# Performance work log

Measured on AMD Instinct MI355X. Metric: run time of the kernel, lower is better.

Reference implementation:

```python
import jax, jax.numpy as jnp
import numpy as np

N = 8192
F_IN = 128
F_OUT = 128
NEG_SLOPE = 0.2


def setup_inputs() -> dict:
    key = jax.random.key(0)
    k_h, k_adj, k_W, k_a = jax.random.split(key, 4)
    h = jax.random.normal(k_h, (N, F_IN), dtype=jnp.float32)
    # binary adjacency mask as float (the module multiplies scores by adj)
    adj = (jax.random.uniform(k_adj, (N, N)) < 0.05).astype(jnp.float32)
    # nn.Linear(in, out, bias=False): weight shape [out, in]
    W = jax.random.normal(k_W, (F_OUT, F_IN), dtype=jnp.float32) / np.sqrt(F_IN)
    # nn.Linear(2*out, 1, bias=False): weight shape [1, 2*out]
    a = jax.random.normal(k_a, (1, 2 * F_OUT), dtype=jnp.float32) / np.sqrt(2 * F_OUT)
    return {"h": h, "adj": adj, "W": W, "a": a}


def reference(h, adj, W, a):
    # Wh: [N, F_out]
    Wh = h @ W.T
    f = Wh.shape[-1]
    # a([Wh_i ; Wh_j]) factored: e[i, j] = leaky_relu(Wh[i]@a1 + Wh[j]@a2)
    a1 = a[0, :f]  # [F_out]
    a2 = a[0, f:]  # [F_out]
    s_i = Wh @ a1  # [N]
    s_j = Wh @ a2  # [N]
    e = jax.nn.leaky_relu(s_i[:, None] + s_j[None, :], NEG_SLOPE)  # [N, N]
    # faithful to original: softmax over dim=1 of e * adj (multiplicative mask)
    attention = jax.nn.softmax(e * adj, axis=1)  # [N, N]
    return attention @ Wh  # [N, F_out]
```

## Files before the change

kernel.cpp:

```cpp
#include <hip/hip_runtime.h>

#define N_NODES 8192
#define FDIM 128
#define NEG_SLOPE 0.2f
#define SEG 512

__global__ __launch_bounds__(256) void wh_fused_kernel(
    const float* __restrict__ h, const float* __restrict__ W,
    float* __restrict__ Wh, float* __restrict__ S) {
  __shared__ float Wt[FDIM * 132];
  __shared__ float rows[32 * 132];
  const int t = threadIdx.x;
  const int base = blockIdx.x * 32;
  for (int it = 0; it < 64; ++it) {
    int idx = t + 256 * it;
    int o = idx >> 7, k = idx & 127;
    Wt[k * 132 + o] = W[idx];
  }
  for (int it = 0; it < 16; ++it) {
    int idx = t + 256 * it;
    int r = idx >> 7, col = idx & 127;
    rows[r * 132 + col] = h[(size_t)base * FDIM + idx];
  }
  __syncthreads();
  const int c4 = (t & 31) * 4;
  const int g = t >> 5;
  float acc[4][4];
#pragma unroll
  for (int rr = 0; rr < 4; ++rr)
#pragma unroll
    for (int cc = 0; cc < 4; ++cc) acc[rr][cc] = 0.f;
  for (int k = 0; k < FDIM; ++k) {
    float4 wv = *(const float4*)&Wt[k * 132 + c4];
    float rv[4];
#pragma unroll
    for (int rr = 0; rr < 4; ++rr) rv[rr] = rows[(4 * g + rr) * 132 + k];
#pragma unroll
    for (int rr = 0; rr < 4; ++rr) {
      acc[rr][0] += rv[rr] * wv.x;
      acc[rr][1] += rv[rr] * wv.y;
      acc[rr][2] += rv[rr] * wv.z;
      acc[rr][3] += rv[rr] * wv.w;
    }
  }
#pragma unroll
  for (int rr = 0; rr < 4; ++rr) {
    int r = base + 4 * g + rr;
    *(float4*)&Wh[(size_t)r * FDIM + c4] =
        make_float4(acc[rr][0], acc[rr][1], acc[rr][2], acc[rr][3]);
  }
  __syncthreads();
  float4 cs = make_float4(acc[0][0] + acc[1][0] + acc[2][0] + acc[3][0],
                          acc[0][1] + acc[1][1] + acc[2][1] + acc[3][1],
                          acc[0][2] + acc[1][2] + acc[2][2] + acc[3][2],
                          acc[0][3] + acc[1][3] + acc[2][3] + acc[3][3]);
  *(float4*)&rows[g * FDIM + c4] = cs;
  __syncthreads();
  if (t < FDIM) {
    float s = 0.f;
#pragma unroll
    for (int gg = 0; gg < 8; ++gg) s += rows[gg * FDIM + t];
    atomicAdd(&S[t], s);
  }
}

__global__ __launch_bounds__(256) void scores_kernel(
    const float* __restrict__ Wh, const float* __restrict__ a,
    float* __restrict__ s1, float* __restrict__ s2) {
  const int t = threadIdx.x;
  const int lane = t & 63;
  const int wave = t >> 6;
  const int row = blockIdx.x * 4 + wave;
  float v0 = Wh[(size_t)row * FDIM + lane];
  float v1 = Wh[(size_t)row * FDIM + 64 + lane];
  float d1 = v0 * a[lane] + v1 * a[64 + lane];
  float d2 = v0 * a[FDIM + lane] + v1 * a[FDIM + 64 + lane];
  for (int off = 32; off; off >>= 1) {
    d1 += __shfl_down(d1, off);
    d2 += __shfl_down(d2, off);
  }
  if (lane == 0) { s1[row] = d1; s2[row] = d2; }
}

__global__ __launch_bounds__(256) void gat_row_kernel(
    const float* __restrict__ adj, const float* __restrict__ Wh,
    const float* __restrict__ s1, const float* __restrict__ s2,
    const float* __restrict__ S, float* __restrict__ out) {
  const int i = blockIdx.x;
  const int t = threadIdx.x;
  const int lane = t & 63;
  const int wave = t >> 6;
  __shared__ float2 pairs[4 * SEG];
  __shared__ int counts[4];
  __shared__ float red[4];
  __shared__ float red2[4];
  __shared__ float fpart[4][FDIM];

  const float s1i = s1[i];
  const float4* __restrict__ arow = (const float4*)(adj + (size_t)i * N_NODES);
  const float4* __restrict__ s2v = (const float4*)s2;
  float2* __restrict__ mypairs = pairs + wave * SEG;
  const unsigned long long lmask = (1ull << lane) - 1ull;

  int cbase = 0;
  float lmax = -1e30f;
  float4 av = arow[t], sv = s2v[t];
#pragma unroll
  for (int it = 0; it < N_NODES / 1024; ++it) {
    float4 avn, svn;
    if (it < N_NODES / 1024 - 1) {
      avn = arow[(it + 1) * 256 + t];
      svn = s2v[(it + 1) * 256 + t];
    }
    const int j4 = it * 256 + t;
    float avv[4] = {av.x, av.y, av.z, av.w};
    float svv[4] = {sv.x, sv.y, sv.z, sv.w};
    float ecand[4];
    bool pred[4];
#pragma unroll
    for (int c = 0; c < 4; ++c) {
      float e = s1i + svv[c];
      e = e > 0.f ? e : NEG_SLOPE * e;
      ecand[c] = e;
      pred[c] = (avv[c] != 0.f);
      if (pred[c]) lmax = fmaxf(lmax, e);
    }
#pragma unroll
    for (int c = 0; c < 4; ++c) {
      unsigned long long b = __ballot(pred[c]);
      if (pred[c]) {
        int pos = cbase + (int)__popcll(b & lmask);
        if (pos < SEG)
          mypairs[pos] = make_float2(ecand[c], __int_as_float(j4 * 4 + c));
      }
      cbase += (int)__popcll(b);
    }
    av = avn; sv = svn;
  }
  if (lane == 0) counts[wave] = cbase < SEG ? cbase : SEG;
  for (int off = 32; off; off >>= 1) lmax = fmaxf(lmax, __shfl_down(lmax, off));
  if (lane == 0) red[wave] = lmax;
  __syncthreads();
  const int cnt = counts[0] + counts[1] + counts[2] + counts[3];
  float m = fmaxf(fmaxf(red[0], red[1]), fmaxf(red[2], red[3]));
  if (cnt < N_NODES) m = fmaxf(m, 0.f);
  const float em = __expf(-m);
  const int mycnt = counts[wave];
  const int half = lane >> 5, lq = lane & 31;
  const float4* __restrict__ Wh4 = (const float4*)Wh;
  float ax = 0.f, ay = 0.f, az = 0.f, aw = 0.f;
  float lsum = 0.f;
  const int nit = (mycnt + 1) >> 1;
  int it = 0;
  for (; it + 1 < nit; it += 2) {
    int p0 = 2 * it + half, p1 = p0 + 2;
    float2 pr0 = mypairs[p0 < mycnt ? p0 : 0];
    float2 pr1 = mypairs[p1 < mycnt ? p1 : 0];
    int j0 = __float_as_int(pr0.y), j1 = __float_as_int(pr1.y);
    float4 v0 = Wh4[(j0 << 5) + lq];
    float4 v1 = Wh4[(j1 << 5) + lq];
    float e0 = __expf(pr0.x - m), e1 = __expf(pr1.x - m);
    bool ok0 = p0 < mycnt, ok1 = p1 < mycnt;
    float w0 = ok0 ? e0 - em : 0.f;
    float w1 = ok1 ? e1 - em : 0.f;
    lsum += (ok0 ? e0 : 0.f) + (ok1 ? e1 : 0.f);
    ax += w0 * v0.x + w1 * v1.x;
    ay += w0 * v0.y + w1 * v1.y;
    az += w0 * v0.z + w1 * v1.z;
    aw += w0 * v0.w + w1 * v1.w;
  }
  if (it < nit) {
    int p0 = 2 * it + half;
    float2 pr0 = mypairs[p0 < mycnt ? p0 : 0];
    int j0 = __float_as_int(pr0.y);
    float4 v0 = Wh4[(j0 << 5) + lq];
    float e0 = __expf(pr0.x - m);
    bool ok0 = p0 < mycnt;
    float w0 = ok0 ? e0 - em : 0.f;
    lsum += ok0 ? e0 : 0.f;
    ax += w0 * v0.x; ay += w0 * v0.y; az += w0 * v0.z; aw += w0 * v0.w;
  }
  ax += __shfl_down(ax, 32);
  ay += __shfl_down(ay, 32);
  az += __shfl_down(az, 32);
  aw += __shfl_down(aw, 32);
  for (int off = 32; off; off >>= 1) lsum += __shfl_down(lsum, off);
  if (lane == 0) red2[wave] = lsum * (1.f / 32.f);
  if (lane < 32)
    *(float4*)&fpart[wave][4 * lq] = make_float4(ax, ay, az, aw);
  __syncthreads();
  if (t < FDIM) {
    float l = red2[0] + red2[1] + red2[2] + red2[3]
              + (float)(N_NODES - cnt) * em;
    float o = (fpart[0][t] + fpart[1][t] + fpart[2][t] + fpart[3][t]
               + em * S[t]) / l;
    out[(size_t)i * FDIM + t] = o;
  }
}

extern "C" void kernel_launch(void* const* d_in, const int* in_sizes, int n_in,
                              void* d_out, int out_size, void* d_ws, size_t ws_size,
                              hipStream_t stream) {
  const float* h   = (const float*)d_in[0];
  const float* adj = (const float*)d_in[1];
  const float* W   = (const float*)d_in[2];
  const float* a   = (const float*)d_in[3];
  float* out = (float*)d_out;
  float* Wh = (float*)d_ws;
  float* s1 = Wh + (size_t)N_NODES * FDIM;
  float* s2 = s1 + N_NODES;
  float* S  = s2 + N_NODES;

  hipMemsetAsync(S, 0, FDIM * sizeof(float), stream);
  hipLaunchKernelGGL(wh_fused_kernel, dim3(N_NODES / 32), dim3(256), 0, stream,
                     h, W, Wh, S);
  hipLaunchKernelGGL(scores_kernel, dim3(N_NODES / 4), dim3(256), 0, stream,
                     Wh, a, s1, s2);
  hipLaunchKernelGGL(gat_row_kernel, dim3(N_NODES), dim3(256), 0, stream,
                     adj, Wh, s1, s2, S, out);
}
```

Measured before the change: 453.9 us.

## Compact adjacency indices first, compute scores and exps only for neighbors

The row kernel now loads all eight adjacency float4 chunks up front and compacts nonzero column indices without reading s2 for every column. Scores are then computed by gathering s2 only at compacted neighbors, exponentials are computed once per neighbor and stored in shared memory, and the aggregation loop is unrolled by four over precomputed weights. This drops the dense s2 stream and redundant exp work, at the cost of an extra pass over shared memory and scattered s2 loads.

```diff
diff --git a/kernel.cpp b/kernel.cpp
--- a/kernel.cpp
+++ b/kernel.cpp
@@ -98,46 +98,39 @@
 
   const float s1i = s1[i];
   const float4* __restrict__ arow = (const float4*)(adj + (size_t)i * N_NODES);
-  const float4* __restrict__ s2v = (const float4*)s2;
   float2* __restrict__ mypairs = pairs + wave * SEG;
   const unsigned long long lmask = (1ull << lane) - 1ull;
 
+  float4 av[8];
+#pragma unroll
+  for (int it = 0; it < 8; ++it) av[it] = arow[it * 256 + t];
   int cbase = 0;
-  float lmax = -1e30f;
-  float4 av = arow[t], sv = s2v[t];
-#pragma unroll
-  for (int it = 0; it < N_NODES / 1024; ++it) {
-    float4 avn, svn;
-    if (it < N_NODES / 1024 - 1) {
-      avn = arow[(it + 1) * 256 + t];
-      svn = s2v[(it + 1) * 256 + t];
-    }
+#pragma unroll
+  for (int it = 0; it < 8; ++it) {
     const int j4 = it * 256 + t;
-    float avv[4] = {av.x, av.y, av.z, av.w};
-    float svv[4] = {sv.x, sv.y, sv.z, sv.w};
-    float ecand[4];
-    bool pred[4];
+    float v[4] = {av[it].x, av[it].y, av[it].z, av[it].w};
 #pragma unroll
     for (int c = 0; c < 4; ++c) {
-      float e = s1i + svv[c];
-      e = e > 0.f ? e : NEG_SLOPE * e;
-      ecand[c] = e;
-      pred[c] = (avv[c] != 0.f);
-      if (pred[c]) lmax = fmaxf(lmax, e);
-    }
-#pragma unroll
-    for (int c = 0; c < 4; ++c) {
-      unsigned long long b = __ballot(pred[c]);
-      if (pred[c]) {
+      bool pred = (v[c] != 0.f);
+      unsigned long long b = __ballot(pred);
+      if (pred) {
         int pos = cbase + (int)__popcll(b & lmask);
-        if (pos < SEG)
-          mypairs[pos] = make_float2(ecand[c], __int_as_float(j4 * 4 + c));
+        if (pos < SEG) ((int*)&mypairs[pos])[1] = j4 * 4 + c;
       }
       cbase += (int)__popcll(b);
     }
-    av = avn; sv = svn;
-  }
-  if (lane == 0) counts[wave] = cbase < SEG ? cbase : SEG;
+  }
+  const int mycnt = cbase < SEG ? cbase : SEG;
+  if (lane == 0) counts[wave] = mycnt;
+
+  float lmax = -1e30f;
+  for (int k = lane; k < mycnt; k += 64) {
+    int j = ((const int*)&mypairs[k])[1];
+    float e = s1i + s2[j];
+    e = e > 0.f ? e : NEG_SLOPE * e;
+    mypairs[k].x = e;
+    lmax = fmaxf(lmax, e);
+  }
   for (int off = 32; off; off >>= 1) lmax = fmaxf(lmax, __shfl_down(lmax, off));
   if (lane == 0) red[wave] = lmax;
   __syncthreads();
@@ -145,47 +138,46 @@
   float m = fmaxf(fmaxf(red[0], red[1]), fmaxf(red[2], red[3]));
   if (cnt < N_NODES) m = fmaxf(m, 0.f);
   const float em = __expf(-m);
-  const int mycnt = counts[wave];
+
+  float lsum = 0.f;
+  for (int k = lane; k < mycnt; k += 64) {
+    float p = __expf(mypairs[k].x - m);
+    mypairs[k].x = p;
+    lsum += p;
+  }
+  for (int off = 32; off; off >>= 1) lsum += __shfl_down(lsum, off);
+  if (lane == 0) red2[wave] = lsum;
+
   const int half = lane >> 5, lq = lane & 31;
   const float4* __restrict__ Wh4 = (const float4*)Wh;
   float ax = 0.f, ay = 0.f, az = 0.f, aw = 0.f;
-  float lsum = 0.f;
   const int nit = (mycnt + 1) >> 1;
   int it = 0;
-  for (; it + 1 < nit; it += 2) {
-    int p0 = 2 * it + half, p1 = p0 + 2;
-    float2 pr0 = mypairs[p0 < mycnt ? p0 : 0];
-    float2 pr1 = mypairs[p1 < mycnt ? p1 : 0];
-    int j0 = __float_as_int(pr0.y), j1 = __float_as_int(pr1.y);
-    float4 v0 = Wh4[(j0 << 5) + lq];
-    float4 v1 = Wh4[(j1 << 5) + lq];
-    float e0 = __expf(pr0.x - m), e1 = __expf(pr1.x - m);
-    bool ok0 = p0 < mycnt, ok1 = p1 < mycnt;
-    float w0 = ok0 ? e0 - em : 0.f;
-    float w1 = ok1 ? e1 - em : 0.f;
-    lsum += (ok0 ? e0 : 0.f) + (ok1 ? e1 : 0.f);
-    ax += w0 * v0.x + w1 * v1.x;
-    ay += w0 * v0.y + w1 * v1.y;
-    az += w0 * v0.z + w1 * v1.z;
-    aw += w0 * v0.w + w1 * v1.w;
-  }
-  if (it < nit) {
-    int p0 = 2 * it + half;
-    float2 pr0 = mypairs[p0 < mycnt ? p0 : 0];
-    int j0 = __float_as_int(pr0.y);
-    float4 v0 = Wh4[(j0 << 5) + lq];
-    float e0 = __expf(pr0.x - m);
-    bool ok0 = p0 < mycnt;
-    float w0 = ok0 ? e0 - em : 0.f;
-    lsum += ok0 ? e0 : 0.f;
-    ax += w0 * v0.x; ay += w0 * v0.y; az += w0 * v0.z; aw += w0 * v0.w;
+  for (; it + 3 < nit; it += 4) {
+#pragma unroll
+    for (int c = 0; c < 4; ++c) {
+      int p = 2 * (it + c) + half;
+      bool ok = p < mycnt;
+      float2 pr = mypairs[ok ? p : 0];
+      int j = ((const int*)&pr)[1];
+      float4 v = Wh4[((size_t)j << 5) + lq];
+      float w = ok ? pr.x - em : 0.f;
+      ax += w * v.x; ay += w * v.y; az += w * v.z; aw += w * v.w;
+    }
+  }
+  for (; it < nit; ++it) {
+    int p = 2 * it + half;
+    bool ok = p < mycnt;
+    float2 pr = mypairs[ok ? p : 0];
+    int j = ((const int*)&pr)[1];
+    float4 v = Wh4[((size_t)j << 5) + lq];
+    float w = ok ? pr.x - em : 0.f;
+    ax += w * v.x; ay += w * v.y; az += w * v.z; aw += w * v.w;
   }
   ax += __shfl_down(ax, 32);
   ay += __shfl_down(ay, 32);
   az += __shfl_down(az, 32);
   aw += __shfl_down(aw, 32);
-  for (int off = 32; off; off >>= 1) lsum += __shfl_down(lsum, off);
-  if (lane == 0) red2[wave] = lsum * (1.f / 32.f);
   if (lane < 32)
     *(float4*)&fpart[wave][4 * lq] = make_float4(ax, ay, az, aw);
   __syncthreads();
```

New measurement: 444.8 us. 2.0% less time.
